# Optimization experiments

Measured on AMD Instinct MI355X. Metric: run time of the kernel, lower is better.

Reference implementation:

```python
import jax, jax.numpy as jnp
import numpy as np

N_DRUG, N_DIS, E, D = 10000, 15000, 1048576, 128

def setup_inputs() -> dict:
    key = jax.random.key(0)
    k = jax.random.split(key, 6)
    return {
        "z_drug": jax.random.normal(k[0], (N_DRUG, D), dtype=jnp.float32),
        "z_disease": jax.random.normal(k[1], (N_DIS, D), dtype=jnp.float32),
        "row": jax.random.randint(k[2], (E,), 0, N_DRUG),
        "col": jax.random.randint(k[3], (E,), 0, N_DIS),
        "W1": jax.random.normal(k[4], (2 * D, D), dtype=jnp.float32) * (1.0 / np.sqrt(2 * D)),
        "b1": jnp.zeros((D,), dtype=jnp.float32),
        "W2": jax.random.normal(k[5], (D, 1), dtype=jnp.float32) * (1.0 / np.sqrt(D)),
        "b2": jnp.zeros((1,), dtype=jnp.float32),
    }

def reference(z_drug, z_disease, row, col, W1, b1, W2, b2):
    # gather per-edge embeddings and concatenate: [E, 2D]
    z = jnp.concatenate([z_drug[row], z_disease[col]], axis=-1)
    h = jax.nn.relu(z @ W1 + b1)          # [E, D]
    out = h @ W2 + b2                      # [E, 1]
    return out.reshape(-1)                 # [E]
```

## Files before the change

kernel.cpp:

```cpp
#include <hip/hip_runtime.h>

typedef __attribute__((ext_vector_type(8))) short short8;
typedef __attribute__((ext_vector_type(4))) float floatx4;
typedef _Float16 half8 __attribute__((ext_vector_type(8)));
typedef _Float16 half4 __attribute__((ext_vector_type(4)));
typedef _Float16 half2v __attribute__((ext_vector_type(2)));

static __device__ __forceinline__ unsigned short f2bf(float x) {
    unsigned int u = __builtin_bit_cast(unsigned int, x);
    unsigned int r = (u + 0x7FFFu + ((u >> 16) & 1u)) >> 16;
    return (unsigned short)r;
}

__global__ void prep_w1(const float* __restrict__ W1, unsigned short* __restrict__ w1t,
                        unsigned* __restrict__ gcur) {
    int i = blockIdx.x * 256 + threadIdx.x;
    int n = i >> 8;
    int k = i & 255;
    w1t[n * 256 + k] = f2bf(W1[k * 128 + n]);
    if (i < 16) gcur[i] = 0;
}

__global__ __launch_bounds__(256, 2) void mid_kernel(
    const float* __restrict__ zd, const float* __restrict__ zs,
    const unsigned short* __restrict__ w1t, const float* __restrict__ b1,
    _Float16* __restrict__ ud, _Float16* __restrict__ us,
    int ndrows, int nsrows, int ntd, int nbg,
    const int* __restrict__ row, const int* __restrict__ col,
    unsigned* __restrict__ gcur, unsigned* __restrict__ rcbuf,
    unsigned* __restrict__ eidbuf, int E)
{
    if ((int)blockIdx.x < nbg) {
        const int tid  = threadIdx.x;
        const int lane = tid & 63;
        const int wave = tid >> 6;
        const int wh   = wave >> 1;
        const int we   = wave & 1;
        const int l15  = lane & 15;
        const int quad = lane >> 4;

        const int b = blockIdx.x;
        const bool isD = (b < ntd);
        const float* __restrict__ z = isD ? zd : zs;
        _Float16* __restrict__ u = isD ? ud : us;
        const int nrows = isD ? ndrows : nsrows;
        const int m0    = (isD ? b : b - ntd) * 64;
        const int koff0 = isD ? 0 : 128;

        short8 wfrag[16];
        #pragma unroll
        for (int s = 0; s < 4; ++s)
            #pragma unroll
            for (int mt = 0; mt < 4; ++mt)
                wfrag[s * 4 + mt] = *reinterpret_cast<const short8*>(
                    &w1t[(size_t)(wh * 64 + mt * 16 + l15) * 256 + koff0 + s * 32 + quad * 8]);

        floatx4 acc[2][4];
        #pragma unroll
        for (int mt = 0; mt < 4; ++mt) {
            floatx4 bb = *reinterpret_cast<const floatx4*>(&b1[wh * 64 + mt * 16 + quad * 4]);
            bb *= 0.5f;
            acc[0][mt] = bb;
            acc[1][mt] = bb;
        }

        int rowi[2], rowc[2];
        #pragma unroll
        for (int et = 0; et < 2; ++et) {
            rowi[et] = m0 + we * 32 + et * 16 + l15;
            rowc[et] = rowi[et] < nrows ? rowi[et] : nrows - 1;
        }

        #pragma unroll
        for (int s = 0; s < 4; ++s) {
            short8 bf[2];
            #pragma unroll
            for (int et = 0; et < 2; ++et) {
                const float* src = &z[(size_t)rowc[et] * 128 + s * 32 + quad * 8];
                floatx4 lo = *reinterpret_cast<const floatx4*>(src);
                floatx4 hi = *reinterpret_cast<const floatx4*>(src + 4);
                short8 t;
                t[0] = (short)f2bf(lo[0]); t[1] = (short)f2bf(lo[1]);
                t[2] = (short)f2bf(lo[2]); t[3] = (short)f2bf(lo[3]);
                t[4] = (short)f2bf(hi[0]); t[5] = (short)f2bf(hi[1]);
                t[6] = (short)f2bf(hi[2]); t[7] = (short)f2bf(hi[3]);
                bf[et] = t;
            }
            #pragma unroll
            for (int et = 0; et < 2; ++et)
                #pragma unroll
                for (int mt = 0; mt < 4; ++mt)
                    acc[et][mt] = __builtin_amdgcn_mfma_f32_16x16x32_bf16(
                        wfrag[s * 4 + mt], bf[et], acc[et][mt], 0, 0, 0);
        }

        #pragma unroll
        for (int et = 0; et < 2; ++et) {
            if (rowi[et] < nrows) {
                #pragma unroll
                for (int mt = 0; mt < 4; ++mt) {
                    half4 hv;
                    #pragma unroll
                    for (int rr = 0; rr < 4; ++rr) hv[rr] = (_Float16)acc[et][mt][rr];
                    *reinterpret_cast<half4*>(
                        &u[(size_t)rowi[et] * 128 + wh * 64 + mt * 16 + quad * 4]) = hv;
                }
            }
        }
    } else {
        __shared__ unsigned wl[4][4];
        __shared__ unsigned gb[4];
        const int tid  = threadIdx.x;
        const int lane = tid & 63;
        const int wave = tid >> 6;
        const int sb   = blockIdx.x - nbg;
        const long base = (long)sb * 2048;

        unsigned rc[8], off[8];
        int cls0, cls1, cls2, cls3, cls4, cls5, cls6, cls7;
        unsigned w0 = 0, w1 = 0, w2c = 0, w3 = 0;

        #pragma unroll
        for (int k = 0; k < 8; ++k) {
            long e = base + wave * 512 + k * 64 + lane;
            int r = row[e], c = col[e];
            rc[k] = (unsigned)r | ((unsigned)c << 14);
            int cl = ((r >= 5000) ? 2 : 0) | ((c >= 7500) ? 1 : 0);
            unsigned long long m0 = __ballot(cl == 0);
            unsigned long long m1 = __ballot(cl == 1);
            unsigned long long m2 = __ballot(cl == 2);
            unsigned long long m3 = __ballot(cl == 3);
            unsigned long long mlt = (1ull << lane) - 1ull;
            unsigned long long mc = (cl == 0) ? m0 : (cl == 1) ? m1 : (cl == 2) ? m2 : m3;
            unsigned wb = (cl == 0) ? w0 : (cl == 1) ? w1 : (cl == 2) ? w2c : w3;
            off[k] = wb + (unsigned)__popcll(mc & mlt);
            w0 += (unsigned)__popcll(m0); w1 += (unsigned)__popcll(m1);
            w2c += (unsigned)__popcll(m2); w3 += (unsigned)__popcll(m3);
            switch (k) {
                case 0: cls0 = cl; break; case 1: cls1 = cl; break;
                case 2: cls2 = cl; break; case 3: cls3 = cl; break;
                case 4: cls4 = cl; break; case 5: cls5 = cl; break;
                case 6: cls6 = cl; break; default: cls7 = cl; break;
            }
        }
        if (lane < 4) {
            unsigned wv = (lane == 0) ? w0 : (lane == 1) ? w1 : (lane == 2) ? w2c : w3;
            wl[wave][lane] = wv;
        }
        __syncthreads();
        if (tid < 4) {
            unsigned tot = wl[0][tid] + wl[1][tid] + wl[2][tid] + wl[3][tid];
            gb[tid] = atomicAdd(&gcur[tid], tot);
        }
        __syncthreads();
        unsigned p0 = 0, p1 = 0, p2 = 0, p3 = 0;
        for (int w = 0; w < 4; ++w)
            if (w < wave) { p0 += wl[w][0]; p1 += wl[w][1]; p2 += wl[w][2]; p3 += wl[w][3]; }

        #pragma unroll
        for (int k = 0; k < 8; ++k) {
            long e = base + wave * 512 + k * 64 + lane;
            int cl = (k == 0) ? cls0 : (k == 1) ? cls1 : (k == 2) ? cls2 : (k == 3) ? cls3
                   : (k == 4) ? cls4 : (k == 5) ? cls5 : (k == 6) ? cls6 : cls7;
            unsigned pre = (cl == 0) ? p0 : (cl == 1) ? p1 : (cl == 2) ? p2 : p3;
            unsigned pos = gb[cl] + pre + off[k];
            rcbuf[(size_t)cl * E + pos]  = rc[k];
            eidbuf[(size_t)cl * E + pos] = (unsigned)e;
        }
    }
}

__global__ __launch_bounds__(256, 8) void edge_eval(
    const _Float16* __restrict__ ud, const _Float16* __restrict__ us,
    const unsigned* __restrict__ gcur, const unsigned* __restrict__ rcbuf,
    const unsigned* __restrict__ eidbuf,
    const float* __restrict__ w2, const float* __restrict__ b2,
    float* __restrict__ out, int E)
{
    const int tid  = threadIdx.x;
    const int lane = tid & 63;
    const int wave = tid >> 6;
    const int le   = lane >> 3;
    const int q    = lane & 7;
    const int lslot = wave * 8 + le;

    const int b    = blockIdx.x;
    const int xcd  = b & 7;
    const int cls  = xcd >> 1;
    const int sub  = ((b >> 3) << 1) | (xcd & 1);
    const int NSUB = (int)((gridDim.x >> 3) << 1);

    const unsigned n = gcur[cls];
    const int nch = (int)((n + 31u) >> 5);
    const unsigned* __restrict__ rcb = rcbuf + (size_t)cls * E;
    const unsigned* __restrict__ eib = eidbuf + (size_t)cls * E;

#if __has_builtin(__builtin_amdgcn_fdot2)
    half2v w2h[8];
    #pragma unroll
    for (int i = 0; i < 2; ++i)
        #pragma unroll
        for (int p = 0; p < 4; ++p) {
            half2v t;
            t[0] = (_Float16)w2[i * 64 + q * 8 + 2 * p];
            t[1] = (_Float16)w2[i * 64 + q * 8 + 2 * p + 1];
            w2h[i * 4 + p] = t;
        }
#else
    float w2r[16];
    #pragma unroll
    for (int i = 0; i < 2; ++i) {
        *reinterpret_cast<floatx4*>(&w2r[i * 8]) =
            *reinterpret_cast<const floatx4*>(&w2[i * 64 + q * 8]);
        *reinterpret_cast<floatx4*>(&w2r[i * 8 + 4]) =
            *reinterpret_cast<const floatx4*>(&w2[i * 64 + q * 8 + 4]);
    }
#endif
    const float b2v = b2[0];

    int t = sub;
    if (t >= nch) return;

    unsigned ei0 = (unsigned)t * 32u + (unsigned)lslot;
    bool v0 = ei0 < n;
    unsigned ci0 = v0 ? ei0 : 0u;
    unsigned rc0 = rcb[ci0];
    unsigned id0 = eib[ci0];

    while (true) {
        const int tn = t + NSUB;

        unsigned r = rc0 & 16383u, c = rc0 >> 14;
        const _Float16* up = ud + (size_t)r * 128 + q * 8;
        const _Float16* vp = us + (size_t)c * 128 + q * 8;
        half8 U0 = *reinterpret_cast<const half8*>(up);
        half8 U1 = *reinterpret_cast<const half8*>(up + 64);
        half8 V0 = *reinterpret_cast<const half8*>(vp);
        half8 V1 = *reinterpret_cast<const half8*>(vp + 64);

        unsigned rc1 = 0, id1 = 0;
        bool v1 = false;
        if (tn < nch) {
            unsigned ei1 = (unsigned)tn * 32u + (unsigned)lslot;
            v1 = ei1 < n;
            unsigned ci1 = v1 ? ei1 : 0u;
            rc1 = rcb[ci1];
            id1 = eib[ci1];
        }

        float acc = 0.f;
        half8 s0 = U0 + V0;
        s0 = __builtin_elementwise_max(s0, (half8)(_Float16)0.f);
        half8 s1 = U1 + V1;
        s1 = __builtin_elementwise_max(s1, (half8)(_Float16)0.f);
#if __has_builtin(__builtin_amdgcn_fdot2)
        #pragma unroll
        for (int p = 0; p < 4; ++p) {
            half2v pr0; pr0[0] = s0[2 * p]; pr0[1] = s0[2 * p + 1];
            acc = __builtin_amdgcn_fdot2(pr0, w2h[p], acc, false);
            half2v pr1; pr1[0] = s1[2 * p]; pr1[1] = s1[2 * p + 1];
            acc = __builtin_amdgcn_fdot2(pr1, w2h[4 + p], acc, false);
        }
#else
        #pragma unroll
        for (int j = 0; j < 8; ++j) {
            acc += (float)s0[j] * w2r[j];
            acc += (float)s1[j] * w2r[8 + j];
        }
#endif
        acc += __shfl_xor(acc, 1);
        acc += __shfl_xor(acc, 2);
        acc += __shfl_xor(acc, 4);
        if (v0 && q == 0) out[id0] = acc + b2v;

        if (tn >= nch) break;
        t = tn; rc0 = rc1; id0 = id1; v0 = v1;
    }
}

extern "C" void kernel_launch(void* const* d_in, const int* in_sizes, int n_in,
                              void* d_out, int out_size, void* d_ws, size_t ws_size,
                              hipStream_t stream) {
    const float* zd = (const float*)d_in[0];
    const float* zs = (const float*)d_in[1];
    const int*   row = (const int*)d_in[2];
    const int*   col = (const int*)d_in[3];
    const float* W1 = (const float*)d_in[4];
    const float* b1 = (const float*)d_in[5];
    const float* w2 = (const float*)d_in[6];
    const float* b2 = (const float*)d_in[7];
    float* out = (float*)d_out;

    const int nd = in_sizes[0];
    const int ns = in_sizes[1];
    const int E  = in_sizes[2];
    const int ndrows = nd / 128;
    const int nsrows = ns / 128;

    unsigned short* w1t = (unsigned short*)d_ws;
    _Float16* ud = (_Float16*)((char*)d_ws + 128 * 256 * sizeof(unsigned short));
    _Float16* us = ud + (size_t)ndrows * 128;
    size_t off = (size_t)((char*)(us + (size_t)nsrows * 128) - (char*)d_ws);
    off = (off + 63) & ~(size_t)63;
    unsigned* gcur   = (unsigned*)((char*)d_ws + off);
    unsigned* rcbuf  = gcur + 16;
    unsigned* eidbuf = rcbuf + (size_t)4 * E;

    hipLaunchKernelGGL(prep_w1, dim3(128), dim3(256), 0, stream, W1, w1t, gcur);

    const int ntd = (ndrows + 63) / 64;
    const int nts = (nsrows + 63) / 64;
    const int nbg = ntd + nts;
    const int nsb = E / 2048;
    hipLaunchKernelGGL(mid_kernel, dim3(nbg + nsb), dim3(256), 0, stream,
                       zd, zs, w1t, b1, ud, us, ndrows, nsrows, ntd, nbg,
                       row, col, gcur, rcbuf, eidbuf, E);

    hipLaunchKernelGGL(edge_eval, dim3(2048), dim3(256), 0, stream,
                       ud, us, gcur, rcbuf, eidbuf, w2, b2, out, E);
}
```

Measured before the change: 122.1 us.

## Bin edges by drug-row block and stage drug embeddings in LDS

Replaces the four-class global scatter with a per-window local counting sort that buckets each 2048-edge window by drug row block (128 rows) and writes a per-window header plus packed 64-bit records. The edge kernel now assigns each block one drug bin, loads that bin's 128 fp16 drug rows into 32KB of shared memory, and walks that bin's segment across windows, so only the disease rows are gathered from global memory. The separate W1 transpose kernel is removed, and each GEMM block converts W1 to bf16 directly with strided loads. The costs are a 32KB LDS footprint at lower occupancy (launch bound 4), short per-window segments that leave many lanes idle, and only 79×12 blocks in the edge kernel.

Result: slower. 143.0 us (+17.1%).

```diff
diff --git a/kernel.cpp b/kernel.cpp
--- a/kernel.cpp
+++ b/kernel.cpp
@@ -12,171 +12,156 @@
     return (unsigned short)r;
 }
 
-__global__ void prep_w1(const float* __restrict__ W1, unsigned short* __restrict__ w1t,
-                        unsigned* __restrict__ gcur) {
-    int i = blockIdx.x * 256 + threadIdx.x;
-    int n = i >> 8;
-    int k = i & 255;
-    w1t[n * 256 + k] = f2bf(W1[k * 128 + n]);
-    if (i < 16) gcur[i] = 0;
-}
-
-__global__ __launch_bounds__(256, 2) void mid_kernel(
+static __device__ void phase_gemm(
+    int b, const float* __restrict__ zd, const float* __restrict__ zs,
+    const float* __restrict__ W1, const float* __restrict__ b1,
+    _Float16* __restrict__ ud, _Float16* __restrict__ us,
+    int ndrows, int nsrows, int ntd)
+{
+    const int tid  = threadIdx.x;
+    const int lane = tid & 63;
+    const int wave = tid >> 6;
+    const int wh   = wave >> 1;
+    const int we   = wave & 1;
+    const int l15  = lane & 15;
+    const int quad = lane >> 4;
+
+    const bool isD = (b < ntd);
+    const float* __restrict__ z = isD ? zd : zs;
+    _Float16* __restrict__ u = isD ? ud : us;
+    const int nrows = isD ? ndrows : nsrows;
+    const int m0    = (isD ? b : b - ntd) * 64;
+    const int koff0 = isD ? 0 : 128;
+    const int whbase = wh * 64;
+
+    short8 wfrag[16];
+    #pragma unroll
+    for (int s = 0; s < 4; ++s)
+        #pragma unroll
+        for (int mt = 0; mt < 4; ++mt) {
+            short8 t;
+            #pragma unroll
+            for (int j = 0; j < 8; ++j)
+                t[j] = (short)f2bf(
+                    W1[(size_t)(koff0 + s * 32 + quad * 8 + j) * 128 +
+                       whbase + mt * 16 + l15]);
+            wfrag[s * 4 + mt] = t;
+        }
+
+    floatx4 acc[2][4];
+    #pragma unroll
+    for (int mt = 0; mt < 4; ++mt) {
+        floatx4 bb = *reinterpret_cast<const floatx4*>(&b1[whbase + mt * 16 + quad * 4]);
+        bb *= 0.5f;
+        acc[0][mt] = bb;
+        acc[1][mt] = bb;
+    }
+
+    int rowi[2], rowc[2];
+    #pragma unroll
+    for (int et = 0; et < 2; ++et) {
+        rowi[et] = m0 + we * 32 + et * 16 + l15;
+        rowc[et] = rowi[et] < nrows ? rowi[et] : nrows - 1;
+    }
+
+    #pragma unroll
+    for (int s = 0; s < 4; ++s) {
+        short8 bf[2];
+        #pragma unroll
+        for (int et = 0; et < 2; ++et) {
+            const float* src = &z[(size_t)rowc[et] * 128 + s * 32 + quad * 8];
+            floatx4 lo = *reinterpret_cast<const floatx4*>(src);
+            floatx4 hi = *reinterpret_cast<const floatx4*>(src + 4);
+            short8 t;
+            t[0] = (short)f2bf(lo[0]); t[1] = (short)f2bf(lo[1]);
+            t[2] = (short)f2bf(lo[2]); t[3] = (short)f2bf(lo[3]);
+            t[4] = (short)f2bf(hi[0]); t[5] = (short)f2bf(hi[1]);
+            t[6] = (short)f2bf(hi[2]); t[7] = (short)f2bf(hi[3]);
+            bf[et] = t;
+        }
+        #pragma unroll
+        for (int et = 0; et < 2; ++et)
+            #pragma unroll
+            for (int mt = 0; mt < 4; ++mt)
+                acc[et][mt] = __builtin_amdgcn_mfma_f32_16x16x32_bf16(
+                    wfrag[s * 4 + mt], bf[et], acc[et][mt], 0, 0, 0);
+    }
+
+    #pragma unroll
+    for (int et = 0; et < 2; ++et) {
+        if (rowi[et] < nrows) {
+            #pragma unroll
+            for (int mt = 0; mt < 4; ++mt) {
+                half4 hv;
+                #pragma unroll
+                for (int rr = 0; rr < 4; ++rr) hv[rr] = (_Float16)acc[et][mt][rr];
+                *reinterpret_cast<half4*>(
+                    &u[(size_t)rowi[et] * 128 + whbase + mt * 16 + quad * 4]) = hv;
+            }
+        }
+    }
+}
+
+static __device__ void phase_scatter(
+    int sb, const int* __restrict__ row, const int* __restrict__ col,
+    unsigned* __restrict__ hdr, unsigned long long* __restrict__ recbuf,
+    int nbins, int hstride)
+{
+    __shared__ unsigned lcnt[160];
+    __shared__ unsigned lbase[161];
+    const int tid = threadIdx.x;
+    for (int i = tid; i < nbins; i += 256) lcnt[i] = 0;
+    __syncthreads();
+
+    const long base = (long)sb * 2048;
+    unsigned rnk[8], rcv[8];
+    int binv[8];
+    #pragma unroll
+    for (int k = 0; k < 8; ++k) {
+        long e = base + k * 256 + tid;
+        int r = row[e], c = col[e];
+        rcv[k] = (unsigned)r | ((unsigned)c << 14);
+        binv[k] = r >> 7;
+        rnk[k] = atomicAdd(&lcnt[binv[k]], 1u);
+    }
+    __syncthreads();
+    if (tid == 0) {
+        unsigned run = 0;
+        for (int i = 0; i < nbins; ++i) { lbase[i] = run; run += lcnt[i]; }
+        lbase[nbins] = run;
+    }
+    __syncthreads();
+    #pragma unroll
+    for (int k = 0; k < 8; ++k) {
+        long e = base + k * 256 + tid;
+        unsigned pos = (unsigned)base + lbase[binv[k]] + rnk[k];
+        recbuf[pos] = (unsigned long long)rcv[k] | ((unsigned long long)(unsigned)e << 32);
+    }
+    for (int i = tid; i <= nbins; i += 256) hdr[(size_t)sb * hstride + i] = lbase[i];
+}
+
+__global__ __launch_bounds__(256, 2) void k_mid(
     const float* __restrict__ zd, const float* __restrict__ zs,
-    const unsigned short* __restrict__ w1t, const float* __restrict__ b1,
+    const float* __restrict__ W1, const float* __restrict__ b1,
     _Float16* __restrict__ ud, _Float16* __restrict__ us,
     int ndrows, int nsrows, int ntd, int nbg,
     const int* __restrict__ row, const int* __restrict__ col,
-    unsigned* __restrict__ gcur, unsigned* __restrict__ rcbuf,
-    unsigned* __restrict__ eidbuf, int E)
+    unsigned* __restrict__ hdr, unsigned long long* __restrict__ recbuf,
+    int nbins, int hstride)
 {
-    if ((int)blockIdx.x < nbg) {
-        const int tid  = threadIdx.x;
-        const int lane = tid & 63;
-        const int wave = tid >> 6;
-        const int wh   = wave >> 1;
-        const int we   = wave & 1;
-        const int l15  = lane & 15;
-        const int quad = lane >> 4;
-
-        const int b = blockIdx.x;
-        const bool isD = (b < ntd);
-        const float* __restrict__ z = isD ? zd : zs;
-        _Float16* __restrict__ u = isD ? ud : us;
-        const int nrows = isD ? ndrows : nsrows;
-        const int m0    = (isD ? b : b - ntd) * 64;
-        const int koff0 = isD ? 0 : 128;
-
-        short8 wfrag[16];
-        #pragma unroll
-        for (int s = 0; s < 4; ++s)
-            #pragma unroll
-            for (int mt = 0; mt < 4; ++mt)
-                wfrag[s * 4 + mt] = *reinterpret_cast<const short8*>(
-                    &w1t[(size_t)(wh * 64 + mt * 16 + l15) * 256 + koff0 + s * 32 + quad * 8]);
-
-        floatx4 acc[2][4];
-        #pragma unroll
-        for (int mt = 0; mt < 4; ++mt) {
-            floatx4 bb = *reinterpret_cast<const floatx4*>(&b1[wh * 64 + mt * 16 + quad * 4]);
-            bb *= 0.5f;
-            acc[0][mt] = bb;
-            acc[1][mt] = bb;
-        }
-
-        int rowi[2], rowc[2];
-        #pragma unroll
-        for (int et = 0; et < 2; ++et) {
-            rowi[et] = m0 + we * 32 + et * 16 + l15;
-            rowc[et] = rowi[et] < nrows ? rowi[et] : nrows - 1;
-        }
-
-        #pragma unroll
-        for (int s = 0; s < 4; ++s) {
-            short8 bf[2];
-            #pragma unroll
-            for (int et = 0; et < 2; ++et) {
-                const float* src = &z[(size_t)rowc[et] * 128 + s * 32 + quad * 8];
-                floatx4 lo = *reinterpret_cast<const floatx4*>(src);
-                floatx4 hi = *reinterpret_cast<const floatx4*>(src + 4);
-                short8 t;
-                t[0] = (short)f2bf(lo[0]); t[1] = (short)f2bf(lo[1]);
-                t[2] = (short)f2bf(lo[2]); t[3] = (short)f2bf(lo[3]);
-                t[4] = (short)f2bf(hi[0]); t[5] = (short)f2bf(hi[1]);
-                t[6] = (short)f2bf(hi[2]); t[7] = (short)f2bf(hi[3]);
-                bf[et] = t;
-            }
-            #pragma unroll
-            for (int et = 0; et < 2; ++et)
-                #pragma unroll
-                for (int mt = 0; mt < 4; ++mt)
-                    acc[et][mt] = __builtin_amdgcn_mfma_f32_16x16x32_bf16(
-                        wfrag[s * 4 + mt], bf[et], acc[et][mt], 0, 0, 0);
-        }
-
-        #pragma unroll
-        for (int et = 0; et < 2; ++et) {
-            if (rowi[et] < nrows) {
-                #pragma unroll
-                for (int mt = 0; mt < 4; ++mt) {
-                    half4 hv;
-                    #pragma unroll
-                    for (int rr = 0; rr < 4; ++rr) hv[rr] = (_Float16)acc[et][mt][rr];
-                    *reinterpret_cast<half4*>(
-                        &u[(size_t)rowi[et] * 128 + wh * 64 + mt * 16 + quad * 4]) = hv;
-                }
-            }
-        }
-    } else {
-        __shared__ unsigned wl[4][4];
-        __shared__ unsigned gb[4];
-        const int tid  = threadIdx.x;
-        const int lane = tid & 63;
-        const int wave = tid >> 6;
-        const int sb   = blockIdx.x - nbg;
-        const long base = (long)sb * 2048;
-
-        unsigned rc[8], off[8];
-        int cls0, cls1, cls2, cls3, cls4, cls5, cls6, cls7;
-        unsigned w0 = 0, w1 = 0, w2c = 0, w3 = 0;
-
-        #pragma unroll
-        for (int k = 0; k < 8; ++k) {
-            long e = base + wave * 512 + k * 64 + lane;
-            int r = row[e], c = col[e];
-            rc[k] = (unsigned)r | ((unsigned)c << 14);
-            int cl = ((r >= 5000) ? 2 : 0) | ((c >= 7500) ? 1 : 0);
-            unsigned long long m0 = __ballot(cl == 0);
-            unsigned long long m1 = __ballot(cl == 1);
-            unsigned long long m2 = __ballot(cl == 2);
-            unsigned long long m3 = __ballot(cl == 3);
-            unsigned long long mlt = (1ull << lane) - 1ull;
-            unsigned long long mc = (cl == 0) ? m0 : (cl == 1) ? m1 : (cl == 2) ? m2 : m3;
-            unsigned wb = (cl == 0) ? w0 : (cl == 1) ? w1 : (cl == 2) ? w2c : w3;
-            off[k] = wb + (unsigned)__popcll(mc & mlt);
-            w0 += (unsigned)__popcll(m0); w1 += (unsigned)__popcll(m1);
-            w2c += (unsigned)__popcll(m2); w3 += (unsigned)__popcll(m3);
-            switch (k) {
-                case 0: cls0 = cl; break; case 1: cls1 = cl; break;
-                case 2: cls2 = cl; break; case 3: cls3 = cl; break;
-                case 4: cls4 = cl; break; case 5: cls5 = cl; break;
-                case 6: cls6 = cl; break; default: cls7 = cl; break;
-            }
-        }
-        if (lane < 4) {
-            unsigned wv = (lane == 0) ? w0 : (lane == 1) ? w1 : (lane == 2) ? w2c : w3;
-            wl[wave][lane] = wv;
-        }
-        __syncthreads();
-        if (tid < 4) {
-            unsigned tot = wl[0][tid] + wl[1][tid] + wl[2][tid] + wl[3][tid];
-            gb[tid] = atomicAdd(&gcur[tid], tot);
-        }
-        __syncthreads();
-        unsigned p0 = 0, p1 = 0, p2 = 0, p3 = 0;
-        for (int w = 0; w < 4; ++w)
-            if (w < wave) { p0 += wl[w][0]; p1 += wl[w][1]; p2 += wl[w][2]; p3 += wl[w][3]; }
-
-        #pragma unroll
-        for (int k = 0; k < 8; ++k) {
-            long e = base + wave * 512 + k * 64 + lane;
-            int cl = (k == 0) ? cls0 : (k == 1) ? cls1 : (k == 2) ? cls2 : (k == 3) ? cls3
-                   : (k == 4) ? cls4 : (k == 5) ? cls5 : (k == 6) ? cls6 : cls7;
-            unsigned pre = (cl == 0) ? p0 : (cl == 1) ? p1 : (cl == 2) ? p2 : p3;
-            unsigned pos = gb[cl] + pre + off[k];
-            rcbuf[(size_t)cl * E + pos]  = rc[k];
-            eidbuf[(size_t)cl * E + pos] = (unsigned)e;
-        }
-    }
-}
-
-__global__ __launch_bounds__(256, 8) void edge_eval(
+    const int b = blockIdx.x;
+    if (b < nbg) phase_gemm(b, zd, zs, W1, b1, ud, us, ndrows, nsrows, ntd);
+    else         phase_scatter(b - nbg, row, col, hdr, recbuf, nbins, hstride);
+}
+
+__global__ __launch_bounds__(256, 4) void k_edge(
     const _Float16* __restrict__ ud, const _Float16* __restrict__ us,
-    const unsigned* __restrict__ gcur, const unsigned* __restrict__ rcbuf,
-    const unsigned* __restrict__ eidbuf,
+    const unsigned* __restrict__ hdr, const unsigned long long* __restrict__ recbuf,
     const float* __restrict__ w2, const float* __restrict__ b2,
-    float* __restrict__ out, int E)
+    float* __restrict__ out, int ndrows, int nbins, int hstride, int nwin, int NW)
 {
+    __shared__ _Float16 uL[128 * 128];
+
     const int tid  = threadIdx.x;
     const int lane = tid & 63;
     const int wave = tid >> 6;
@@ -184,16 +169,17 @@
     const int q    = lane & 7;
     const int lslot = wave * 8 + le;
 
-    const int b    = blockIdx.x;
-    const int xcd  = b & 7;
-    const int cls  = xcd >> 1;
-    const int sub  = ((b >> 3) << 1) | (xcd & 1);
-    const int NSUB = (int)((gridDim.x >> 3) << 1);
-
-    const unsigned n = gcur[cls];
-    const int nch = (int)((n + 31u) >> 5);
-    const unsigned* __restrict__ rcb = rcbuf + (size_t)cls * E;
-    const unsigned* __restrict__ eib = eidbuf + (size_t)cls * E;
+    const int b   = blockIdx.x;
+    const int bin = b % nbins;
+    const int w   = b / nbins;
+
+    const int r0 = bin << 7;
+    int nr = ndrows - r0; if (nr > 128) nr = 128;
+    for (int i = tid; i < nr * 16; i += 256) {
+        int rr = i >> 4, pp = i & 15;
+        *reinterpret_cast<half8*>(&uL[rr * 128 + pp * 8]) =
+            *reinterpret_cast<const half8*>(&ud[(size_t)(r0 + rr) * 128 + pp * 8]);
+    }
 
 #if __has_builtin(__builtin_amdgcn_fdot2)
     half2v w2h[8];
@@ -217,64 +203,66 @@
     }
 #endif
     const float b2v = b2[0];
-
-    int t = sub;
-    if (t >= nch) return;
-
-    unsigned ei0 = (unsigned)t * 32u + (unsigned)lslot;
-    bool v0 = ei0 < n;
-    unsigned ci0 = v0 ? ei0 : 0u;
-    unsigned rc0 = rcb[ci0];
-    unsigned id0 = eib[ci0];
+    __syncthreads();
+
+    int sb = w;
+    if (sb >= nwin) return;
+    unsigned h0 = hdr[(size_t)sb * hstride + bin];
+    unsigned h1 = hdr[(size_t)sb * hstride + bin + 1];
 
     while (true) {
-        const int tn = t + NSUB;
-
-        unsigned r = rc0 & 16383u, c = rc0 >> 14;
-        const _Float16* up = ud + (size_t)r * 128 + q * 8;
-        const _Float16* vp = us + (size_t)c * 128 + q * 8;
-        half8 U0 = *reinterpret_cast<const half8*>(up);
-        half8 U1 = *reinterpret_cast<const half8*>(up + 64);
-        half8 V0 = *reinterpret_cast<const half8*>(vp);
-        half8 V1 = *reinterpret_cast<const half8*>(vp + 64);
-
-        unsigned rc1 = 0, id1 = 0;
-        bool v1 = false;
-        if (tn < nch) {
-            unsigned ei1 = (unsigned)tn * 32u + (unsigned)lslot;
-            v1 = ei1 < n;
-            unsigned ci1 = v1 ? ei1 : 0u;
-            rc1 = rcb[ci1];
-            id1 = eib[ci1];
-        }
-
-        float acc = 0.f;
-        half8 s0 = U0 + V0;
-        s0 = __builtin_elementwise_max(s0, (half8)(_Float16)0.f);
-        half8 s1 = U1 + V1;
-        s1 = __builtin_elementwise_max(s1, (half8)(_Float16)0.f);
+        const int sbn = sb + NW;
+        unsigned hn0 = 0, hn1 = 0;
+        if (sbn < nwin) {
+            hn0 = hdr[(size_t)sbn * hstride + bin];
+            hn1 = hdr[(size_t)sbn * hstride + bin + 1];
+        }
+
+        const unsigned segbase = (unsigned)sb * 2048u + h0;
+        const int seg = (int)(h1 - h0);
+
+        for (int t0 = 0; t0 < seg; t0 += 32) {
+            const int idx = t0 + lslot;
+            const bool vld = idx < seg;
+            const unsigned long long rec = recbuf[segbase + (vld ? idx : 0)];
+            const unsigned rl = (unsigned)rec & 127u;
+            const unsigned c  = ((unsigned)rec >> 14) & 16383u;
+
+            const _Float16* vp = us + (size_t)c * 128 + q * 8;
+            const half8 V0 = *reinterpret_cast<const half8*>(vp);
+            const half8 V1 = *reinterpret_cast<const half8*>(vp + 64);
+            const _Float16* up = &uL[rl * 128 + q * 8];
+            const half8 U0 = *reinterpret_cast<const half8*>(up);
+            const half8 U1 = *reinterpret_cast<const half8*>(up + 64);
+
+            float acc = 0.f;
+            half8 s0 = U0 + V0;
+            s0 = __builtin_elementwise_max(s0, (half8)(_Float16)0.f);
+            half8 s1 = U1 + V1;
+            s1 = __builtin_elementwise_max(s1, (half8)(_Float16)0.f);
 #if __has_builtin(__builtin_amdgcn_fdot2)
-        #pragma unroll
-        for (int p = 0; p < 4; ++p) {
-            half2v pr0; pr0[0] = s0[2 * p]; pr0[1] = s0[2 * p + 1];
-            acc = __builtin_amdgcn_fdot2(pr0, w2h[p], acc, false);
-            half2v pr1; pr1[0] = s1[2 * p]; pr1[1] = s1[2 * p + 1];
-            acc = __builtin_amdgcn_fdot2(pr1, w2h[4 + p], acc, false);
-        }
+            #pragma unroll
+            for (int p = 0; p < 4; ++p) {
+                half2v pr0; pr0[0] = s0[2 * p]; pr0[1] = s0[2 * p + 1];
+                acc = __builtin_amdgcn_fdot2(pr0, w2h[p], acc, false);
+                half2v pr1; pr1[0] = s1[2 * p]; pr1[1] = s1[2 * p + 1];
+                acc = __builtin_amdgcn_fdot2(pr1, w2h[4 + p], acc, false);
+            }
 #else
-        #pragma unroll
-        for (int j = 0; j < 8; ++j) {
-            acc += (float)s0[j] * w2r[j];
-            acc += (float)s1[j] * w2r[8 + j];
-        }
+            #pragma unroll
+            for (int j = 0; j < 8; ++j) {
+                acc += (float)s0[j] * w2r[j];
+                acc += (float)s1[j] * w2r[8 + j];
+            }
 #endif
-        acc += __shfl_xor(acc, 1);
-        acc += __shfl_xor(acc, 2);
-        acc += __shfl_xor(acc, 4);
-        if (v0 && q == 0) out[id0] = acc + b2v;
-
-        if (tn >= nch) break;
-        t = tn; rc0 = rc1; id0 = id1; v0 = v1;
+            acc += __shfl_xor(acc, 1);
+            acc += __shfl_xor(acc, 2);
+            acc += __shfl_xor(acc, 4);
+            if (vld && q == 0) out[(unsigned)(rec >> 32)] = acc + b2v;
+        }
+
+        if (sbn >= nwin) break;
+        sb = sbn; h0 = hn0; h1 = hn1;
     }
 }
 
@@ -297,25 +285,27 @@
     const int ndrows = nd / 128;
     const int nsrows = ns / 128;
 
-    unsigned short* w1t = (unsigned short*)d_ws;
-    _Float16* ud = (_Float16*)((char*)d_ws + 128 * 256 * sizeof(unsigned short));
+    const int nbins   = (ndrows + 127) >> 7;
+    const int hstride = nbins + 1;
+    const int nwin    = E / 2048;
+
+    _Float16* ud = (_Float16*)d_ws;
     _Float16* us = ud + (size_t)ndrows * 128;
     size_t off = (size_t)((char*)(us + (size_t)nsrows * 128) - (char*)d_ws);
     off = (off + 63) & ~(size_t)63;
-    unsigned* gcur   = (unsigned*)((char*)d_ws + off);
-    unsigned* rcbuf  = gcur + 16;
-    unsigned* eidbuf = rcbuf + (size_t)4 * E;
-
-    hipLaunchKernelGGL(prep_w1, dim3(128), dim3(256), 0, stream, W1, w1t, gcur);
+    unsigned* hdr = (unsigned*)((char*)d_ws + off);
+    unsigned long long* recbuf = (unsigned long long*)
+        (((uintptr_t)(hdr + (size_t)nwin * hstride) + 63) & ~(uintptr_t)63);
 
     const int ntd = (ndrows + 63) / 64;
     const int nts = (nsrows + 63) / 64;
     const int nbg = ntd + nts;
-    const int nsb = E / 2048;
-    hipLaunchKernelGGL(mid_kernel, dim3(nbg + nsb), dim3(256), 0, stream,
-                       zd, zs, w1t, b1, ud, us, ndrows, nsrows, ntd, nbg,
-                       row, col, gcur, rcbuf, eidbuf, E);
-
-    hipLaunchKernelGGL(edge_eval, dim3(2048), dim3(256), 0, stream,
-                       ud, us, gcur, rcbuf, eidbuf, w2, b2, out, E);
-}
+    hipLaunchKernelGGL(k_mid, dim3(nbg + nwin), dim3(256), 0, stream,
+                       zd, zs, W1, b1, ud, us, ndrows, nsrows, ntd, nbg,
+                       row, col, hdr, recbuf, nbins, hstride);
+
+    const int NW = 12;
+    hipLaunchKernelGGL(k_edge, dim3(nbins * NW), dim3(256), 0, stream,
+                       ud, us, hdr, recbuf, w2, b2, out,
+                       ndrows, nbins, hstride, nwin, NW);
+}
```

## Drop W1 prep kernel, pack edge records into 64-bit entries

Applied to the files above, without the earlier changes.

Removes the separate W1 transpose/convert kernel. Each GEMM block now reads and converts its W1 fragments straight from fp32 global memory with strided scalar loads, and a memset clears the counters. The row/col pair and the edge id are packed into one 64-bit record, so edge_eval issues one load per edge instead of two from separate buffers. Binning now uses tid-contiguous edge indexing and half-split thresholds computed from the table sizes. This saves a launch and some memory traffic, but adds uncoalesced W1 reads in every GEMM block.

Result: no change. 123.4 us (+1.1%).

```diff
diff --git a/kernel.cpp b/kernel.cpp
--- a/kernel.cpp
+++ b/kernel.cpp
@@ -12,23 +12,14 @@
     return (unsigned short)r;
 }
 
-__global__ void prep_w1(const float* __restrict__ W1, unsigned short* __restrict__ w1t,
-                        unsigned* __restrict__ gcur) {
-    int i = blockIdx.x * 256 + threadIdx.x;
-    int n = i >> 8;
-    int k = i & 255;
-    w1t[n * 256 + k] = f2bf(W1[k * 128 + n]);
-    if (i < 16) gcur[i] = 0;
-}
-
 __global__ __launch_bounds__(256, 2) void mid_kernel(
     const float* __restrict__ zd, const float* __restrict__ zs,
-    const unsigned short* __restrict__ w1t, const float* __restrict__ b1,
+    const float* __restrict__ W1, const float* __restrict__ b1,
     _Float16* __restrict__ ud, _Float16* __restrict__ us,
     int ndrows, int nsrows, int ntd, int nbg,
     const int* __restrict__ row, const int* __restrict__ col,
-    unsigned* __restrict__ gcur, unsigned* __restrict__ rcbuf,
-    unsigned* __restrict__ eidbuf, int E)
+    unsigned* __restrict__ gcur, unsigned long long* __restrict__ recbuf,
+    int E, int rowh, int colh)
 {
     if ((int)blockIdx.x < nbg) {
         const int tid  = threadIdx.x;
@@ -46,19 +37,26 @@
         const int nrows = isD ? ndrows : nsrows;
         const int m0    = (isD ? b : b - ntd) * 64;
         const int koff0 = isD ? 0 : 128;
+        const int whbase = wh * 64;
 
         short8 wfrag[16];
         #pragma unroll
         for (int s = 0; s < 4; ++s)
             #pragma unroll
-            for (int mt = 0; mt < 4; ++mt)
-                wfrag[s * 4 + mt] = *reinterpret_cast<const short8*>(
-                    &w1t[(size_t)(wh * 64 + mt * 16 + l15) * 256 + koff0 + s * 32 + quad * 8]);
+            for (int mt = 0; mt < 4; ++mt) {
+                short8 t;
+                #pragma unroll
+                for (int j = 0; j < 8; ++j)
+                    t[j] = (short)f2bf(
+                        W1[(size_t)(koff0 + s * 32 + quad * 8 + j) * 128 +
+                           whbase + mt * 16 + l15]);
+                wfrag[s * 4 + mt] = t;
+            }
 
         floatx4 acc[2][4];
         #pragma unroll
         for (int mt = 0; mt < 4; ++mt) {
-            floatx4 bb = *reinterpret_cast<const floatx4*>(&b1[wh * 64 + mt * 16 + quad * 4]);
+            floatx4 bb = *reinterpret_cast<const floatx4*>(&b1[whbase + mt * 16 + quad * 4]);
             bb *= 0.5f;
             acc[0][mt] = bb;
             acc[1][mt] = bb;
@@ -103,7 +101,7 @@
                     #pragma unroll
                     for (int rr = 0; rr < 4; ++rr) hv[rr] = (_Float16)acc[et][mt][rr];
                     *reinterpret_cast<half4*>(
-                        &u[(size_t)rowi[et] * 128 + wh * 64 + mt * 16 + quad * 4]) = hv;
+                        &u[(size_t)rowi[et] * 128 + whbase + mt * 16 + quad * 4]) = hv;
                 }
             }
         }
@@ -122,10 +120,10 @@
 
         #pragma unroll
         for (int k = 0; k < 8; ++k) {
-            long e = base + wave * 512 + k * 64 + lane;
+            long e = base + k * 256 + tid;
             int r = row[e], c = col[e];
             rc[k] = (unsigned)r | ((unsigned)c << 14);
-            int cl = ((r >= 5000) ? 2 : 0) | ((c >= 7500) ? 1 : 0);
+            int cl = ((r >= rowh) ? 2 : 0) | ((c >= colh) ? 1 : 0);
             unsigned long long m0 = __ballot(cl == 0);
             unsigned long long m1 = __ballot(cl == 1);
             unsigned long long m2 = __ballot(cl == 2);
@@ -159,21 +157,20 @@
 
         #pragma unroll
         for (int k = 0; k < 8; ++k) {
-            long e = base + wave * 512 + k * 64 + lane;
+            long e = base + k * 256 + tid;
             int cl = (k == 0) ? cls0 : (k == 1) ? cls1 : (k == 2) ? cls2 : (k == 3) ? cls3
                    : (k == 4) ? cls4 : (k == 5) ? cls5 : (k == 6) ? cls6 : cls7;
             unsigned pre = (cl == 0) ? p0 : (cl == 1) ? p1 : (cl == 2) ? p2 : p3;
             unsigned pos = gb[cl] + pre + off[k];
-            rcbuf[(size_t)cl * E + pos]  = rc[k];
-            eidbuf[(size_t)cl * E + pos] = (unsigned)e;
+            recbuf[(size_t)cl * E + pos] =
+                (unsigned long long)rc[k] | ((unsigned long long)(unsigned)e << 32);
         }
     }
 }
 
 __global__ __launch_bounds__(256, 8) void edge_eval(
     const _Float16* __restrict__ ud, const _Float16* __restrict__ us,
-    const unsigned* __restrict__ gcur, const unsigned* __restrict__ rcbuf,
-    const unsigned* __restrict__ eidbuf,
+    const unsigned* __restrict__ gcur, const unsigned long long* __restrict__ recbuf,
     const float* __restrict__ w2, const float* __restrict__ b2,
     float* __restrict__ out, int E)
 {
@@ -192,8 +189,7 @@
 
     const unsigned n = gcur[cls];
     const int nch = (int)((n + 31u) >> 5);
-    const unsigned* __restrict__ rcb = rcbuf + (size_t)cls * E;
-    const unsigned* __restrict__ eib = eidbuf + (size_t)cls * E;
+    const unsigned long long* __restrict__ recb = recbuf + (size_t)cls * E;
 
 #if __has_builtin(__builtin_amdgcn_fdot2)
     half2v w2h[8];
@@ -223,14 +219,13 @@
 
     unsigned ei0 = (unsigned)t * 32u + (unsigned)lslot;
     bool v0 = ei0 < n;
-    unsigned ci0 = v0 ? ei0 : 0u;
-    unsigned rc0 = rcb[ci0];
-    unsigned id0 = eib[ci0];
+    unsigned long long rec0 = recb[v0 ? ei0 : 0u];
 
     while (true) {
         const int tn = t + NSUB;
 
-        unsigned r = rc0 & 16383u, c = rc0 >> 14;
+        unsigned r = (unsigned)rec0 & 16383u;
+        unsigned c = ((unsigned)rec0 >> 14) & 16383u;
         const _Float16* up = ud + (size_t)r * 128 + q * 8;
         const _Float16* vp = us + (size_t)c * 128 + q * 8;
         half8 U0 = *reinterpret_cast<const half8*>(up);
@@ -238,14 +233,12 @@
         half8 V0 = *reinterpret_cast<const half8*>(vp);
         half8 V1 = *reinterpret_cast<const half8*>(vp + 64);
 
-        unsigned rc1 = 0, id1 = 0;
+        unsigned long long rec1 = 0;
         bool v1 = false;
         if (tn < nch) {
             unsigned ei1 = (unsigned)tn * 32u + (unsigned)lslot;
             v1 = ei1 < n;
-            unsigned ci1 = v1 ? ei1 : 0u;
-            rc1 = rcb[ci1];
-            id1 = eib[ci1];
+            rec1 = recb[v1 ? ei1 : 0u];
         }
 
         float acc = 0.f;
@@ -271,10 +264,10 @@
         acc += __shfl_xor(acc, 1);
         acc += __shfl_xor(acc, 2);
         acc += __shfl_xor(acc, 4);
-        if (v0 && q == 0) out[id0] = acc + b2v;
+        if (v0 && q == 0) out[(unsigned)(rec0 >> 32)] = acc + b2v;
 
         if (tn >= nch) break;
-        t = tn; rc0 = rc1; id0 = id1; v0 = v1;
+        t = tn; rec0 = rec1; v0 = v1;
     }
 }
 
@@ -296,26 +289,26 @@
     const int E  = in_sizes[2];
     const int ndrows = nd / 128;
     const int nsrows = ns / 128;
-
-    unsigned short* w1t = (unsigned short*)d_ws;
-    _Float16* ud = (_Float16*)((char*)d_ws + 128 * 256 * sizeof(unsigned short));
+    const int rowh = ndrows >> 1;
+    const int colh = nsrows >> 1;
+
+    _Float16* ud = (_Float16*)d_ws;
     _Float16* us = ud + (size_t)ndrows * 128;
     size_t off = (size_t)((char*)(us + (size_t)nsrows * 128) - (char*)d_ws);
     off = (off + 63) & ~(size_t)63;
-    unsigned* gcur   = (unsigned*)((char*)d_ws + off);
-    unsigned* rcbuf  = gcur + 16;
-    unsigned* eidbuf = rcbuf + (size_t)4 * E;
-
-    hipLaunchKernelGGL(prep_w1, dim3(128), dim3(256), 0, stream, W1, w1t, gcur);
+    unsigned* gcur = (unsigned*)((char*)d_ws + off);
+    unsigned long long* recbuf = (unsigned long long*)((char*)gcur + 64);
+
+    hipMemsetAsync(gcur, 0, 16 * sizeof(unsigned), stream);
 
     const int ntd = (ndrows + 63) / 64;
     const int nts = (nsrows + 63) / 64;
     const int nbg = ntd + nts;
     const int nsb = E / 2048;
     hipLaunchKernelGGL(mid_kernel, dim3(nbg + nsb), dim3(256), 0, stream,
-                       zd, zs, w1t, b1, ud, us, ndrows, nsrows, ntd, nbg,
-                       row, col, gcur, rcbuf, eidbuf, E);
+                       zd, zs, W1, b1, ud, us, ndrows, nsrows, ntd, nbg,
+                       row, col, gcur, recbuf, E, rowh, colh);
 
     hipLaunchKernelGGL(edge_eval, dim3(2048), dim3(256), 0, stream,
-                       ud, us, gcur, rcbuf, eidbuf, w2, b2, out, E);
+                       ud, us, gcur, recbuf, w2, b2, out, E);
 }
```
